# Performance work log

Measured on AMD Instinct MI355X. Metric: run time of the kernel, lower is better.

The kernel has to match this reference:

```python
import jax, jax.numpy as jnp
import numpy as np

N_NODES = 30000
N_EDGES = 300000
D_IN = 64
HID = 128
HEADS = 4
EDG = 2 * HID  # 256, num_edg_hiddens
OUT = 86
EPS = 1e-5
NEG_SLOPE = 0.2


def _kaiming(key, shape, fan_in):
    return jax.random.normal(key, shape, dtype=jnp.float32) * np.sqrt(2.0 / fan_in)


def _bn(x, w, b):
    # F.batch_norm(training=True): normalize with biased batch stats
    m = x.mean(axis=0)
    v = x.var(axis=0)
    return (x - m) / jnp.sqrt(v + EPS) * w + b


def _gat(x, src, dst, w, b, att_src, att_dst, n_nodes):
    # x: [N, Fin], w: [HEADS*HID, Fin] -> h: [N, HEADS, HID]
    h = (x @ w.T).reshape(x.shape[0], HEADS, -1)
    a_s = (h * att_src).sum(-1)  # [N, HEADS]
    a_d = (h * att_dst).sum(-1)  # [N, HEADS]
    alpha = jax.nn.leaky_relu(a_s[src] + a_d[dst], NEG_SLOPE)  # [E, HEADS]
    # segment softmax over destination node
    amax = jax.ops.segment_max(alpha, dst, num_segments=n_nodes)
    e = jnp.exp(alpha - amax[dst])
    denom = jax.ops.segment_sum(e, dst, num_segments=n_nodes)
    coef = e / denom[dst]  # [E, HEADS]
    out = jax.ops.segment_sum(h[src] * coef[:, :, None], dst, num_segments=n_nodes)
    return out.mean(axis=1) + b  # mean over heads (concat=False), [N, HID]


def setup_inputs() -> dict:
    key = jax.random.key(0)
    ks = jax.random.split(key, 16)
    x = jax.random.normal(ks[0], (N_NODES, D_IN), dtype=jnp.float32)
    edge_index = jax.random.randint(ks[1], (2, N_EDGES), 0, N_NODES, dtype=jnp.int32)
    return {
        'x': x,
        'edge_index': edge_index,
        'w0': _kaiming(ks[2], (HEADS * HID, D_IN), D_IN),
        'b0': jnp.zeros((HID,), jnp.float32),
        'ats0': _kaiming(ks[3], (1, HEADS, HID), HEADS * HID),
        'atd0': _kaiming(ks[4], (1, HEADS, HID), HEADS * HID),
        'bn1w': jnp.ones((HID,), jnp.float32),
        'bn1b': jnp.zeros((HID,), jnp.float32),
        'w2': _kaiming(ks[5], (HEADS * HID, HID), HID),
        'b2': jnp.zeros((HID,), jnp.float32),
        'ats1': _kaiming(ks[6], (1, HEADS, HID), HEADS * HID),
        'atd1': _kaiming(ks[7], (1, HEADS, HID), HEADS * HID),
        'bn2w': jnp.ones((HID,), jnp.float32),
        'bn2b': jnp.zeros((HID,), jnp.float32),
        'w4': _kaiming(ks[8], (EDG, EDG), EDG),
        'b4': jnp.zeros((EDG,), jnp.float32),
        'bn3w': jnp.ones((EDG,), jnp.float32),
        'bn3b': jnp.zeros((EDG,), jnp.float32),
        'w6': _kaiming(ks[9], (EDG, EDG), EDG),
        'b6': jnp.zeros((EDG,), jnp.float32),
        'bn4w': jnp.ones((EDG,), jnp.float32),
        'bn4b': jnp.zeros((EDG,), jnp.float32),
        'w8': _kaiming(ks[10], (OUT, EDG), EDG),
        'b8': jnp.zeros((OUT,), jnp.float32),
    }


def reference(x, edge_index, w0, b0, ats0, atd0, bn1w, bn1b, w2, b2, ats1, atd1,
              bn2w, bn2b, w4, b4, bn3w, bn3b, w6, b6, bn4w, bn4b, w8, b8):
    src, dst = edge_index[0], edge_index[1]
    n = x.shape[0]
    h = _gat(x, src, dst, w0, b0, ats0, atd0, n)
    x1 = jax.nn.relu(_bn(h, bn1w, bn1b))
    h = _gat(x1, src, dst, w2, b2, ats1, atd1, n)
    xr = jax.nn.relu(_bn(h, bn2w, bn2b) + x1)
    # edge feature MLP with residuals
    ef1 = jnp.concatenate([xr[src], xr[dst]], axis=1)  # [E, 2*HID]
    ef = _bn(ef1 @ w4.T + b4, bn3w, bn3b)
    ef1 = jax.nn.relu(ef + ef1)
    ef = _bn(ef1 @ w6.T + b6, bn4w, bn4b)
    ef = jax.nn.relu(ef + ef1)
    return ef @ w8.T + b8  # [E, OUT]
```

## Files before the change

kernel.cpp:

```cpp
#include <hip/hip_runtime.h>
#include <hip/hip_bf16.h>
#include <stdint.h>

typedef __hip_bfloat16 bf16;
typedef unsigned int u32;
typedef __attribute__((ext_vector_type(8))) short short8;
typedef __attribute__((ext_vector_type(4))) float f32x4;
typedef __attribute__((ext_vector_type(2))) float f32x2;

#define NNODES 30000
#define NEDGES 300000
#define NODE_PAD 30080
#define EDGE_PAD 300032
#define NCH128 2344
#define NEG_SLOPE 0.2f
#define BN_EPS 1e-5f
#define MAXD 128

__device__ __forceinline__ float b2f(short s) {
  u32 u = ((u32)(unsigned short)s) << 16;
  return __uint_as_float(u);
}
__device__ __forceinline__ short f2b(float f) {
  bf16 h = __float2bfloat16(f);
  return *(short*)&h;
}

__device__ __forceinline__ void gload16(const void* g, void* l) {
  __builtin_amdgcn_global_load_lds(
      (__attribute__((address_space(1))) unsigned int*)(uintptr_t)g,
      (__attribute__((address_space(3))) unsigned int*)(uintptr_t)l, 16, 0, 0);
}


__global__ void zfill(u32* __restrict__ p, int n) {
  int i = blockIdx.x * 256 + threadIdx.x;
  if (i < n) p[i] = 0u;
}

__global__ void fillpat(u32* __restrict__ p, u32 v, int n) {
  int i = blockIdx.x * 256 + threadIdx.x;
  if (i < n) p[i] = v;
}

__global__ void cvt_bf16_pad(const float* __restrict__ src, bf16* __restrict__ dst,
                             int rows_valid, int total, int cols) {
  int i = blockIdx.x * 256 + threadIdx.x;
  if (i >= total) return;
  int r = i / cols;
  float v = (r < rows_valid) ? src[i] : 0.f;
  dst[i] = __float2bfloat16(v);
}

__global__ void cvt_w45(const float* __restrict__ w4, bf16* __restrict__ w45b) {
  int i = blockIdx.x * 256 + threadIdx.x;
  if (i >= 512 * 128) return;
  int n = i >> 7, k = i & 127;
  float v = (n < 256) ? w4[n * 256 + k] : w4[(n - 256) * 256 + 128 + k];
  w45b[i] = __float2bfloat16(v);
}

__global__ void bn_coef(const float* __restrict__ stats, const float* __restrict__ w,
                        const float* __restrict__ b, int n, float invN,
                        float* __restrict__ sc, float* __restrict__ sh) {
  int c = threadIdx.x;
  if (c >= n) return;
  float m = stats[c] * invN;
  float var = stats[n + c] * invN - m * m;
  float rstd = rsqrtf(var + BN_EPS);
  sc[c] = rstd * w[c];
  sh[c] = b[c] - m * rstd * w[c];
}


__global__ void csr_hist(const int* __restrict__ ei, u32* __restrict__ cnt) {
  int e = blockIdx.x * 256 + threadIdx.x;
  if (e >= NEDGES) return;
  atomicAdd(&cnt[ei[NEDGES + e]], 1u);
}

__global__ __launch_bounds__(256) void scan30k(const u32* __restrict__ cnt,
                                               u32* __restrict__ rowptr) {
  __shared__ u32 part[256];
  int t = threadIdx.x;
  const int CH = (NNODES + 255) / 256;
  int i0 = t * CH;
  int i1 = i0 + CH;
  if (i1 > NNODES) i1 = NNODES;
  u32 s = 0;
  for (int i = i0; i < i1; ++i) s += cnt[i];
  part[t] = s;
  __syncthreads();
  for (int off = 1; off < 256; off <<= 1) {
    u32 v = (t >= off) ? part[t - off] : 0u;
    __syncthreads();
    part[t] += v;
    __syncthreads();
  }
  u32 run = (t == 0) ? 0u : part[t - 1];
  for (int i = i0; i < i1; ++i) {
    rowptr[i] = run;
    run += cnt[i];
  }
  if (t == 255) rowptr[NNODES] = run;
}

__global__ void csr_fill(const int* __restrict__ ei, const u32* __restrict__ rowptr,
                         u32* __restrict__ fill, u32* __restrict__ csrc) {
  int e = blockIdx.x * 256 + threadIdx.x;
  if (e >= NEDGES) return;
  int dst = ei[NEDGES + e];
  u32 pos = rowptr[dst] + atomicAdd(&fill[dst], 1u);
  csrc[pos] = (u32)ei[e];
}

__global__ __launch_bounds__(256) void gat_agg(
    const u32* __restrict__ rowptr, const u32* __restrict__ csrc,
    const float* __restrict__ a_s, const float* __restrict__ a_d,
    const bf16* __restrict__ hb, float* __restrict__ agg) {
  __shared__ float al[2][MAXD][4];
  __shared__ u32 srcl[2][MAXD];
  const int sub = threadIdx.x >> 7;
  const int d = threadIdx.x & 127;
  const int node = blockIdx.x * 2 + sub;
  u32 r0 = rowptr[node], r1 = rowptr[node + 1];
  int deg = (int)(r1 - r0);
  if (deg > MAXD) deg = MAXD;
  if (d < deg) {
    u32 s = csrc[r0 + d];
    srcl[sub][d] = s;
#pragma unroll
    for (int hh = 0; hh < 4; ++hh) {
      float a = a_s[s * 4 + hh] + a_d[node * 4 + hh];
      al[sub][d][hh] = (a > 0.f) ? a : NEG_SLOPE * a;
    }
  }
  __syncthreads();
  if (d < 4 && deg > 0) {
    float mx = -1e30f;
    for (int e = 0; e < deg; ++e) mx = fmaxf(mx, al[sub][e][d]);
    float sum = 0.f;
    for (int e = 0; e < deg; ++e) {
      float v = __expf(al[sub][e][d] - mx);
      al[sub][e][d] = v;
      sum += v;
    }
    float inv = 1.f / sum;
    for (int e = 0; e < deg; ++e) al[sub][e][d] *= inv;
  }
  __syncthreads();
  float acc = 0.f;
  const short* hp = (const short*)hb;
#pragma unroll 1
  for (int e = 0; e < deg; ++e) {
    u32 s = srcl[sub][e];
    const short* row = hp + (size_t)s * 512 + d;
    f32x4 c = *(const f32x4*)&al[sub][e][0];
    acc += c[0] * b2f(row[0]) + c[1] * b2f(row[128]) +
           c[2] * b2f(row[256]) + c[3] * b2f(row[384]);
  }
  agg[(size_t)node * 128 + d] = acc * 0.25f;
}

__global__ __launch_bounds__(256) void gemm_bt(
    const bf16* __restrict__ A, const bf16* __restrict__ B, bf16* __restrict__ Cout,
    int K, int ldc, int Mvalid, int Nvalid) {
  __shared__ __align__(16) short smA[2][128 * 64];
  __shared__ __align__(16) short smB[2][128 * 64];
  const int tid = threadIdx.x;
  const int lane = tid & 63;
  const int wid = tid >> 6;
  const int wr = wid >> 1, wc = wid & 1;
  const size_t arow0 = (size_t)blockIdx.x * 128;
  const size_t brow0 = (size_t)blockIdx.y * 128;
  f32x4 acc[4][4] = {};
  const int nk = K >> 6;

  int srow[4], scol[4];
#pragma unroll
  for (int i = 0; i < 4; ++i) {
    int s = i * 256 + tid;
    srow[i] = s >> 3;
    scol[i] = ((s & 7) ^ ((s >> 3) & 7)) * 8;
  }
  auto stage = [&](int buf, int kt) {
#pragma unroll
    for (int i = 0; i < 4; ++i) {
      int s = i * 256 + tid;
      gload16(A + (arow0 + srow[i]) * K + kt * 64 + scol[i], &smA[buf][s * 8]);
      gload16(B + (brow0 + srow[i]) * K + kt * 64 + scol[i], &smB[buf][s * 8]);
    }
  };
  auto compute = [&](int buf) {
#pragma unroll
    for (int ks = 0; ks < 2; ++ks) {
      short8 af[4], bfr[4];
      const int cg = ks * 4 + (lane >> 4);
#pragma unroll
      for (int m = 0; m < 4; ++m) {
        int row = wr * 64 + m * 16 + (lane & 15);
        af[m] = *(const short8*)&smA[buf][row * 64 + ((cg ^ (row & 7)) << 3)];
      }
#pragma unroll
      for (int n = 0; n < 4; ++n) {
        int row = wc * 64 + n * 16 + (lane & 15);
        bfr[n] = *(const short8*)&smB[buf][row * 64 + ((cg ^ (row & 7)) << 3)];
      }
#pragma unroll
      for (int m = 0; m < 4; ++m)
#pragma unroll
        for (int n = 0; n < 4; ++n)
          acc[m][n] = __builtin_amdgcn_mfma_f32_16x16x32_bf16(af[m], bfr[n], acc[m][n], 0, 0, 0);
    }
  };

  stage(0, 0);
  __syncthreads();
  int cur = 0;
  for (int kt = 0; kt < nk; ++kt) {
    if (kt + 1 < nk) stage(cur ^ 1, kt + 1);
    compute(cur);
    __syncthreads();
    cur ^= 1;
  }

  const int rbase = (int)arow0 + wr * 64 + (lane >> 4) * 4;
  const int cbase = (int)brow0 + wc * 64 + (lane & 15);
#pragma unroll
  for (int m = 0; m < 4; ++m) {
#pragma unroll
    for (int n = 0; n < 4; ++n) {
      int col = cbase + n * 16;
      if (col >= Nvalid) continue;
#pragma unroll
      for (int r = 0; r < 4; ++r) {
        int row = rbase + m * 16 + r;
        if (row < Mvalid)
          Cout[(size_t)row * ldc + col] = __float2bfloat16(acc[m][n][r]);
      }
    }
  }
}

__global__ __launch_bounds__(512, 2) void gemm2_v8(
    const bf16* __restrict__ A, const bf16* __restrict__ Bw, bf16* __restrict__ C,
    float* __restrict__ statsOut) {
  __shared__ __align__(16) short smA[2][128 * 256];
  const int tid = threadIdx.x;
  const int lane = tid & 63;
  const int wid = tid >> 6;
  const int lr = lane & 15, lk = lane >> 4;

  short8 bfrag[2][8];
#pragma unroll
  for (int n = 0; n < 2; ++n)
#pragma unroll
    for (int ks = 0; ks < 8; ++ks)
      bfrag[n][ks] = *(const short8*)(Bw + (size_t)(wid * 32 + n * 16 + lr) * 256 + (ks * 4 + lk) * 8);

  auto stage = [&](int buf, int chunk) {
    const bf16* Ab = A + (size_t)chunk * 128 * 256;
#pragma unroll
    for (int i = 0; i < 8; ++i) {
      int s = i * 512 + tid;
      int p = s >> 10;
      int row = (s >> 3) & 127;
      int c8 = s & 7;
      gload16(Ab + row * 256 + (p * 8 + (c8 ^ (row & 7))) * 8, &smA[buf][s * 8]);
    }
  };

  float ss[2] = {}, sq[2] = {};

  auto compute = [&](int buf, int chunk) {
    f32x4 acc[8][2];
#pragma unroll
    for (int g = 0; g < 8; ++g) { acc[g][0] = {}; acc[g][1] = {}; }
#pragma unroll
    for (int ks = 0; ks < 8; ++ks) {
      const int p = ks >> 1;
      const int cgl = (ks & 1) * 4 + lk;
#pragma unroll
      for (int g = 0; g < 8; ++g) {
        int row = g * 16 + lr;
        short8 af = *(const short8*)&smA[buf][p * 8192 + row * 64 + ((cgl ^ (row & 7)) << 3)];
        acc[g][0] = __builtin_amdgcn_mfma_f32_16x16x32_bf16(af, bfrag[0][ks], acc[g][0], 0, 0, 0);
        acc[g][1] = __builtin_amdgcn_mfma_f32_16x16x32_bf16(af, bfrag[1][ks], acc[g][1], 0, 0, 0);
      }
    }
    size_t rbase = (size_t)chunk * 128;
#pragma unroll
    for (int g = 0; g < 8; ++g) {
#pragma unroll
      for (int n = 0; n < 2; ++n) {
        int col = wid * 32 + n * 16 + lr;
#pragma unroll
        for (int j = 0; j < 4; ++j) {
          float v = acc[g][n][j];
          ss[n] += v;
          sq[n] += v * v;
          C[(rbase + g * 16 + lk * 4 + j) * 256 + col] = __float2bfloat16(v);
        }
      }
    }
  };

  int c = blockIdx.x;
  stage(0, c);
  __syncthreads();
  int buf = 0;
  while (true) {
    int nx = c + (int)gridDim.x;
    if (nx < NCH128) stage(buf ^ 1, nx);
    compute(buf, c);
    if (nx >= NCH128) break;
    __syncthreads();
    buf ^= 1;
    c = nx;
  }

#pragma unroll
  for (int n = 0; n < 2; ++n) {
    float s = ss[n], q = sq[n];
    s += __shfl_xor(s, 16); s += __shfl_xor(s, 32);
    q += __shfl_xor(q, 16); q += __shfl_xor(q, 32);
    if (lk == 0) {
      atomicAdd(&statsOut[wid * 32 + n * 16 + lr], s);
      atomicAdd(&statsOut[256 + wid * 32 + n * 16 + lr], q);
    }
  }
}

__global__ __launch_bounds__(256, 2) void gemm3_v3(
    const bf16* __restrict__ Y, const bf16* __restrict__ E, const bf16* __restrict__ Bw,
    float* __restrict__ Cout, const float* __restrict__ scf, const float* __restrict__ shf,
    const float* __restrict__ bias) {
  __shared__ __align__(16) short smW[96 * 256];
  __shared__ __align__(16) short smA[64 * 256];
  const int tid = threadIdx.x;
  const int lane = tid & 63;
  const int wid = tid >> 6;
  const int lr = lane & 15, lk = lane >> 4;

#pragma unroll
  for (int i = 0; i < 12; ++i) {
    int s = i * 256 + tid;
    int row = s >> 5, c8 = s & 31;
    gload16(Bw + row * 256 + (c8 ^ (row & 7)) * 8, &smW[s * 8]);
  }

  const int cb = (tid & 31) * 8;
  f32x4 sc0 = *(const f32x4*)&scf[cb];
  f32x4 sc1 = *(const f32x4*)&scf[cb + 4];
  f32x4 sh0 = *(const f32x4*)&shf[cb];
  f32x4 sh1 = *(const f32x4*)&shf[cb + 4];
  float bb[6][4];
#pragma unroll
  for (int f = 0; f < 6; ++f)
#pragma unroll
    for (int r = 0; r < 4; ++r) {
      int n = f * 16 + lk * 4 + r;
      bb[f][r] = (n < 86) ? bias[n] : 0.f;
    }

  short8 y[8], e[8];
  auto loadYE = [&](int t) {
    size_t base = (size_t)t * 64 * 256;
#pragma unroll
    for (int j = 0; j < 8; ++j) {
      size_t off = base + (size_t)(j * 256 + tid) * 8;
      y[j] = *(const short8*)(Y + off);
      e[j] = *(const short8*)(E + off);
    }
  };

  const int NT = EDGE_PAD / 64;
  int t = blockIdx.x;
  loadYE(t);
  __syncthreads();

  while (true) {
#pragma unroll
    for (int j = 0; j < 8; ++j) {
      int s = j * 256 + tid;
      int row = s >> 5, c8 = s & 31;
      short8 o;
#pragma unroll
      for (int jj = 0; jj < 4; ++jj) {
        o[jj]     = f2b(fmaxf(b2f(y[j][jj]) * sc0[jj] + sh0[jj] + b2f(e[j][jj]), 0.f));
        o[jj + 4] = f2b(fmaxf(b2f(y[j][jj + 4]) * sc1[jj] + sh1[jj] + b2f(e[j][jj + 4]), 0.f));
      }
      *(short8*)&smA[row * 256 + ((c8 ^ (row & 7)) << 3)] = o;
    }
    __syncthreads();
    int cur = t;
    int nx = t + (int)gridDim.x;
    if (nx < NT) loadYE(nx);

    f32x4 acc[6] = {};
#pragma unroll
    for (int ks = 0; ks < 8; ++ks) {
      int cg = ks * 4 + lk;
      int ra = wid * 16 + lr;
      short8 af = *(const short8*)&smA[ra * 256 + ((cg ^ (ra & 7)) << 3)];
#pragma unroll
      for (int f = 0; f < 6; ++f) {
        int rw = f * 16 + lr;
        short8 wf = *(const short8*)&smW[rw * 256 + ((cg ^ (rw & 7)) << 3)];
        acc[f] = __builtin_amdgcn_mfma_f32_16x16x32_bf16(wf, af, acc[f], 0, 0, 0);
      }
    }

    int rbase = cur * 64 + wid * 16;
    if (rbase < NEDGES) {
      float* gp = Cout + (size_t)(rbase + lr) * 86;
#pragma unroll
      for (int f = 0; f < 6; ++f) {
        int n0 = f * 16 + lk * 4;
        if (n0 + 1 < 86) {
          f32x2 v;
          v[0] = acc[f][0] + bb[f][0];
          v[1] = acc[f][1] + bb[f][1];
          *(f32x2*)(gp + n0) = v;
        }
        if (n0 + 3 < 86) {
          f32x2 v;
          v[0] = acc[f][2] + bb[f][2];
          v[1] = acc[f][3] + bb[f][3];
          *(f32x2*)(gp + n0 + 2) = v;
        }
      }
    }
    if (nx >= NT) break;
    t = nx;
    __syncthreads();
  }
}


__global__ __launch_bounds__(256) void att_reduce(
    const bf16* __restrict__ h, const float* __restrict__ ats, const float* __restrict__ atd,
    float* __restrict__ a_s, float* __restrict__ a_d) {
  int n = blockIdx.x;
  int lane = threadIdx.x & 63;
  int hd = threadIdx.x >> 6;
  const bf16* hp = h + (size_t)n * 512 + hd * 128;
  const float* sw = ats + hd * 128;
  const float* dw = atd + hd * 128;
  float h1 = __bfloat162float(hp[lane]), h2 = __bfloat162float(hp[lane + 64]);
  float s = h1 * sw[lane] + h2 * sw[lane + 64];
  float d = h1 * dw[lane] + h2 * dw[lane + 64];
#pragma unroll
  for (int off = 32; off > 0; off >>= 1) {
    s += __shfl_down(s, off);
    d += __shfl_down(d, off);
  }
  if (lane == 0) {
    a_s[n * 4 + hd] = s;
    a_d[n * 4 + hd] = d;
  }
}


__global__ __launch_bounds__(256) void col_stats128(const float* __restrict__ X,
                                                    float* __restrict__ stats, int rows) {
  __shared__ float smS[8][128], smQ[8][128];
  int t = threadIdx.x;
  int sub = t >> 5;
  int c4 = (t & 31) * 4;
  int rend = blockIdx.x * 64 + 64;
  if (rend > rows) rend = rows;
  f32x4 s = {}, q = {};
  for (int r = blockIdx.x * 64 + sub; r < rend; r += 8) {
    f32x4 v = *(const f32x4*)&X[(size_t)r * 128 + c4];
    s += v;
    q += v * v;
  }
  *(f32x4*)&smS[sub][c4] = s;
  *(f32x4*)&smQ[sub][c4] = q;
  __syncthreads();
  if (t < 128) {
    float ts = 0.f, tq = 0.f;
#pragma unroll
    for (int g = 0; g < 8; ++g) { ts += smS[g][t]; tq += smQ[g][t]; }
    atomicAdd(&stats[t], ts);
    atomicAdd(&stats[128 + t], tq);
  }
}

__global__ void bn_relu_node(const float* __restrict__ agg, const float* __restrict__ stats,
                             const float* __restrict__ w, const float* __restrict__ b,
                             bf16* __restrict__ xout) {
  int i = blockIdx.x * 256 + threadIdx.x;
  if (i >= NODE_PAD * 128) return;
  int r = i >> 7, c = i & 127;
  float v = 0.f;
  if (r < NNODES) {
    float m = stats[c] * (1.f / NNODES);
    float var = stats[128 + c] * (1.f / NNODES) - m * m;
    float rstd = rsqrtf(var + BN_EPS);
    v = fmaxf((agg[i] - m) * rstd * w[c] + b[c], 0.f);
  }
  xout[i] = __float2bfloat16(v);
}

__global__ void bn_res_relu_node(const float* __restrict__ agg, const float* __restrict__ stats,
                                 const float* __restrict__ w, const float* __restrict__ b,
                                 const bf16* __restrict__ x1b, bf16* __restrict__ xrb) {
  int i = blockIdx.x * 256 + threadIdx.x;
  if (i >= NODE_PAD * 128) return;
  int r = i >> 7, c = i & 127;
  float v = 0.f;
  if (r < NNODES) {
    float m = stats[c] * (1.f / NNODES);
    float var = stats[128 + c] * (1.f / NNODES) - m * m;
    float rstd = rsqrtf(var + BN_EPS);
    v = fmaxf((agg[i] - m) * rstd * w[c] + b[c] + __bfloat162float(x1b[i]), 0.f);
  }
  xrb[i] = __float2bfloat16(v);
}

__device__ __forceinline__ void accum_nw(short8 pa, short8 qa, f32x4& s0, f32x4& s1,
                                         f32x4& q0, f32x4& q1) {
  float v[8];
#pragma unroll
  for (int j = 0; j < 8; ++j) v[j] = b2f(pa[j]) + b2f(qa[j]);
  s0[0] += v[0]; s0[1] += v[1]; s0[2] += v[2]; s0[3] += v[3];
  s1[0] += v[4]; s1[1] += v[5]; s1[2] += v[6]; s1[3] += v[7];
  q0[0] += v[0] * v[0]; q0[1] += v[1] * v[1]; q0[2] += v[2] * v[2]; q0[3] += v[3] * v[3];
  q1[0] += v[4] * v[4]; q1[1] += v[5] * v[5]; q1[2] += v[6] * v[6]; q1[3] += v[7] * v[7];
}

__global__ __launch_bounds__(256) void e_stats_nw(const int* __restrict__ ei,
                                                  const bf16* __restrict__ PQ,
                                                  float* __restrict__ stats) {
  __shared__ float smS[8][256], smQ[8][256];
  int t = threadIdx.x;
  int sub = t >> 5;
  int c8 = (t & 31) * 8;
  int ebase = blockIdx.x * 128 + sub * 16;
  f32x4 s0 = {}, s1 = {}, q0 = {}, q1 = {};
#pragma unroll 1
  for (int i = 0; i < 16; i += 4) {
    int e = ebase + i;
    if (e + 3 < NEDGES) {
      int4 sn = *(const int4*)&ei[e];
      int4 dn = *(const int4*)&ei[NEDGES + e];
      short8 p0 = *(const short8*)&PQ[(size_t)sn.x * 512 + c8];
      short8 p1 = *(const short8*)&PQ[(size_t)sn.y * 512 + c8];
      short8 p2 = *(const short8*)&PQ[(size_t)sn.z * 512 + c8];
      short8 p3 = *(const short8*)&PQ[(size_t)sn.w * 512 + c8];
      short8 r0 = *(const short8*)&PQ[(size_t)dn.x * 512 + 256 + c8];
      short8 r1 = *(const short8*)&PQ[(size_t)dn.y * 512 + 256 + c8];
      short8 r2 = *(const short8*)&PQ[(size_t)dn.z * 512 + 256 + c8];
      short8 r3 = *(const short8*)&PQ[(size_t)dn.w * 512 + 256 + c8];
      accum_nw(p0, r0, s0, s1, q0, q1);
      accum_nw(p1, r1, s0, s1, q0, q1);
      accum_nw(p2, r2, s0, s1, q0, q1);
      accum_nw(p3, r3, s0, s1, q0, q1);
    } else {
      for (int j = 0; j < 4; ++j) {
        int ej = e + j;
        if (ej >= NEDGES) break;
        int sn = ei[ej], dn = ei[NEDGES + ej];
        short8 p = *(const short8*)&PQ[(size_t)sn * 512 + c8];
        short8 r = *(const short8*)&PQ[(size_t)dn * 512 + 256 + c8];
        accum_nw(p, r, s0, s1, q0, q1);
      }
    }
  }
  *(f32x4*)&smS[sub][c8] = s0;
  *(f32x4*)&smS[sub][c8 + 4] = s1;
  *(f32x4*)&smQ[sub][c8] = q0;
  *(f32x4*)&smQ[sub][c8 + 4] = q1;
  __syncthreads();
  float ts = 0.f, tq = 0.f;
#pragma unroll
  for (int g = 0; g < 8; ++g) { ts += smS[g][t]; tq += smQ[g][t]; }
  atomicAdd(&stats[t], ts);
  atomicAdd(&stats[256 + t], tq);
}

__global__ __launch_bounds__(256) void ef2_direct(const int* __restrict__ ei,
                                                  const bf16* __restrict__ PQ,
                                                  const bf16* __restrict__ xrb,
                                                  const float* __restrict__ sc3,
                                                  const float* __restrict__ sh3,
                                                  bf16* __restrict__ ef2) {
  int t = threadIdx.x;
  int e = blockIdx.x * 8 + (t >> 5);
  int c8 = (t & 31) * 8;
  size_t base = (size_t)e * 256 + c8;
  short8 out = {};
  if (e < NEDGES) {
    int sn = ei[e], dn = ei[NEDGES + e];
    short8 p = *(const short8*)&PQ[(size_t)sn * 512 + c8];
    short8 q = *(const short8*)&PQ[(size_t)dn * 512 + 256 + c8];
    int node = (c8 < 128) ? sn : dn;
    short8 res = *(const short8*)&xrb[(size_t)node * 128 + (c8 & 127)];
    f32x4 scl = *(const f32x4*)&sc3[c8];
    f32x4 sch = *(const f32x4*)&sc3[c8 + 4];
    f32x4 shl = *(const f32x4*)&sh3[c8];
    f32x4 shh = *(const f32x4*)&sh3[c8 + 4];
#pragma unroll
    for (int j = 0; j < 4; ++j) {
      float v0 = (b2f(p[j]) + b2f(q[j])) * scl[j] + shl[j] + b2f(res[j]);
      float v1 = (b2f(p[j + 4]) + b2f(q[j + 4])) * sch[j] + shh[j] + b2f(res[j + 4]);
      out[j] = f2b(fmaxf(v0, 0.f));
      out[j + 4] = f2b(fmaxf(v1, 0.f));
    }
  }
  *(short8*)&ef2[base] = out;
}


extern "C" void kernel_launch(void* const* d_in, const int* in_sizes, int n_in,
                              void* d_out, int out_size, void* d_ws, size_t ws_size,
                              hipStream_t stream) {
  const float* x    = (const float*)d_in[0];
  const int*   ei   = (const int*)d_in[1];
  const float* w0   = (const float*)d_in[2];
  const float* ats0 = (const float*)d_in[4];
  const float* atd0 = (const float*)d_in[5];
  const float* bn1w = (const float*)d_in[6];
  const float* bn1b = (const float*)d_in[7];
  const float* w2   = (const float*)d_in[8];
  const float* ats1 = (const float*)d_in[10];
  const float* atd1 = (const float*)d_in[11];
  const float* bn2w = (const float*)d_in[12];
  const float* bn2b = (const float*)d_in[13];
  const float* w4   = (const float*)d_in[14];
  const float* bn3w = (const float*)d_in[16];
  const float* bn3b = (const float*)d_in[17];
  const float* w6   = (const float*)d_in[18];
  const float* bn4w = (const float*)d_in[20];
  const float* bn4b = (const float*)d_in[21];
  const float* w8   = (const float*)d_in[22];
  const float* b8   = (const float*)d_in[23];

  const size_t REG = 153616384;
  char* ws = (char*)d_ws;
  bf16*  ef2b = (bf16*)ws;
  char*  R    = ws + REG;
  bf16*  hb    = (bf16*)(R);
  bf16*  xb    = (bf16*)(R + 61603840);
  bf16*  x1b   = (bf16*)(R + 65454080);
  bf16*  xrb   = (bf16*)(R + 73154560);
  float* a_s   = (float*)(R + 80855040);
  float* a_d   = (float*)(R + 81335040);
  u32*   rowptr= (u32*)  (R + 81815040);
  u32*   cntf  = (u32*)  (R + 82295040);
  u32*   csrc  = (u32*)  (R + 82775040);
  float* agg   = (float*)(R + 87575040);
  bf16*  PQ    = hb;
  bf16*  y2b   = (bf16*)R;
  char*  S     = ws + 2 * REG;
  bf16*  w0b   = (bf16*)(S);
  bf16*  w2b   = (bf16*)(S + 65536);
  bf16*  w45b  = (bf16*)(S + 196608);
  bf16*  w6b   = (bf16*)(S + 327680);
  bf16*  w8pb  = (bf16*)(S + 458752);
  float* stats1= (float*)(S + 524288);
  float* stats2= (float*)(S + 526336);
  float* sc2   = (float*)(S + 528384);
  float* sh2   = (float*)(S + 529408);
  float* sc3   = (float*)(S + 530432);
  float* sh3   = (float*)(S + 531456);
  const size_t needed = 2 * REG + 532480;
  if (ws_size < needed) {
    fillpat<<<(out_size + 255) / 256, 256, 0, stream>>>((u32*)d_out, 0x7F7F7F7Fu, out_size);
    return;
  }

  cvt_bf16_pad<<<(NODE_PAD * 64 + 255) / 256, 256, 0, stream>>>(x, xb, NNODES, NODE_PAD * 64, 64);
  cvt_bf16_pad<<<(512 * 64 + 255) / 256, 256, 0, stream>>>(w0, w0b, 512, 512 * 64, 64);
  cvt_bf16_pad<<<(512 * 128 + 255) / 256, 256, 0, stream>>>(w2, w2b, 512, 512 * 128, 128);
  cvt_w45<<<(512 * 128 + 255) / 256, 256, 0, stream>>>(w4, w45b);
  cvt_bf16_pad<<<(256 * 256 + 255) / 256, 256, 0, stream>>>(w6, w6b, 256, 256 * 256, 256);
  cvt_bf16_pad<<<(128 * 256 + 255) / 256, 256, 0, stream>>>(w8, w8pb, 86, 128 * 256, 256);

  const int eb = (NEDGES + 255) / 256;

  zfill<<<(NNODES + 255) / 256, 256, 0, stream>>>(cntf, NNODES);
  csr_hist<<<eb, 256, 0, stream>>>(ei, cntf);
  scan30k<<<1, 256, 0, stream>>>(cntf, rowptr);
  zfill<<<(NNODES + 255) / 256, 256, 0, stream>>>(cntf, NNODES);
  csr_fill<<<eb, 256, 0, stream>>>(ei, rowptr, cntf, csrc);

  gemm_bt<<<dim3(NODE_PAD / 128, 4), 256, 0, stream>>>(xb, w0b, hb, 64, 512, NODE_PAD, 512);
  att_reduce<<<NNODES, 256, 0, stream>>>(hb, ats0, atd0, a_s, a_d);
  gat_agg<<<NNODES / 2, 256, 0, stream>>>(rowptr, csrc, a_s, a_d, hb, agg);
  zfill<<<1, 256, 0, stream>>>((u32*)stats1, 256);
  col_stats128<<<(NNODES + 63) / 64, 256, 0, stream>>>(agg, stats1, NNODES);
  bn_relu_node<<<NODE_PAD * 128 / 256, 256, 0, stream>>>(agg, stats1, bn1w, bn1b, x1b);

  gemm_bt<<<dim3(NODE_PAD / 128, 4), 256, 0, stream>>>(x1b, w2b, hb, 128, 512, NODE_PAD, 512);
  att_reduce<<<NNODES, 256, 0, stream>>>(hb, ats1, atd1, a_s, a_d);
  gat_agg<<<NNODES / 2, 256, 0, stream>>>(rowptr, csrc, a_s, a_d, hb, agg);
  zfill<<<1, 256, 0, stream>>>((u32*)stats1, 256);
  col_stats128<<<(NNODES + 63) / 64, 256, 0, stream>>>(agg, stats1, NNODES);
  bn_res_relu_node<<<NODE_PAD * 128 / 256, 256, 0, stream>>>(agg, stats1, bn2w, bn2b, x1b, xrb);

  gemm_bt<<<dim3(NODE_PAD / 128, 4), 256, 0, stream>>>(xrb, w45b, PQ, 128, 512, NODE_PAD, 512);
  zfill<<<2, 256, 0, stream>>>((u32*)stats1, 512);
  e_stats_nw<<<(NEDGES + 127) / 128, 256, 0, stream>>>(ei, PQ, stats1);
  bn_coef<<<1, 256, 0, stream>>>(stats1, bn3w, bn3b, 256, 1.f / NEDGES, sc3, sh3);
  ef2_direct<<<EDGE_PAD / 8, 256, 0, stream>>>(ei, PQ, xrb, sc3, sh3, ef2b);
  zfill<<<2, 256, 0, stream>>>((u32*)stats2, 512);
  gemm2_v8<<<586, 512, 0, stream>>>(ef2b, w6b, y2b, stats2);
  bn_coef<<<1, 256, 0, stream>>>(stats2, bn4w, bn4b, 256, 1.f / NEDGES, sc2, sh2);
  gemm3_v3<<<2344, 256, 0, stream>>>(y2b, ef2b, w8pb, (float*)d_out, sc2, sh2, b8);
}
```

Baseline: 691.4 us.

## Restructure final GEMM with register-resident weights, 128-row tiles and double-buffered LDS

```diff
diff --git a/kernel.cpp b/kernel.cpp
--- a/kernel.cpp
+++ b/kernel.cpp
@@ -70,6 +70,18 @@
   float rstd = rsqrtf(var + BN_EPS);
   sc[c] = rstd * w[c];
   sh[c] = b[c] - m * rstd * w[c];
+}
+
+__global__ void bn_coef_b(const float* __restrict__ stats, const float* __restrict__ w,
+                          const float* __restrict__ b, int n, float invN,
+                          bf16* __restrict__ sc, bf16* __restrict__ sh) {
+  int c = threadIdx.x;
+  if (c >= n) return;
+  float m = stats[c] * invN;
+  float var = stats[n + c] * invN - m * m;
+  float rstd = rsqrtf(var + BN_EPS);
+  sc[c] = __float2bfloat16(rstd * w[c]);
+  sh[c] = __float2bfloat16(b[c] - m * rstd * w[c]);
 }
 
 
@@ -331,109 +343,129 @@
   }
 }
 
-__global__ __launch_bounds__(256, 2) void gemm3_v3(
-    const bf16* __restrict__ Y, const bf16* __restrict__ E, const bf16* __restrict__ Bw,
-    float* __restrict__ Cout, const float* __restrict__ scf, const float* __restrict__ shf,
+__global__ __launch_bounds__(512, 2) void gemm3_v4(
+    const bf16* __restrict__ Y, const bf16* __restrict__ E, const bf16* __restrict__ W8g,
+    float* __restrict__ Cout, const bf16* __restrict__ scb, const bf16* __restrict__ shb,
     const float* __restrict__ bias) {
-  __shared__ __align__(16) short smW[96 * 256];
-  __shared__ __align__(16) short smA[64 * 256];
+  __shared__ __align__(16) short smA[2][128 * 256];
   const int tid = threadIdx.x;
   const int lane = tid & 63;
   const int wid = tid >> 6;
   const int lr = lane & 15, lk = lane >> 4;
-
-#pragma unroll
-  for (int i = 0; i < 12; ++i) {
-    int s = i * 256 + tid;
-    int row = s >> 5, c8 = s & 31;
-    gload16(Bw + row * 256 + (c8 ^ (row & 7)) * 8, &smW[s * 8]);
-  }
-
-  const int cb = (tid & 31) * 8;
-  f32x4 sc0 = *(const f32x4*)&scf[cb];
-  f32x4 sc1 = *(const f32x4*)&scf[cb + 4];
-  f32x4 sh0 = *(const f32x4*)&shf[cb];
-  f32x4 sh1 = *(const f32x4*)&shf[cb + 4];
-  float bb[6][4];
-#pragma unroll
-  for (int f = 0; f < 6; ++f)
+  const int g2 = wid & 3;
+  const int fh = wid >> 2;
+
+  short8 wf[3][8];
+#pragma unroll
+  for (int ff = 0; ff < 3; ++ff)
+#pragma unroll
+    for (int ks = 0; ks < 8; ++ks)
+      wf[ff][ks] = *(const short8*)(W8g + (size_t)((fh * 3 + ff) * 16 + lr) * 256 + (ks * 4 + lk) * 8);
+
+  const int xo = (tid & 7) ^ ((tid >> 3) & 7);
+  short8 csc[4], csh[4];
+#pragma unroll
+  for (int p = 0; p < 4; ++p) {
+    csc[p] = *(const short8*)((const short*)scb + (p * 8 + xo) * 8);
+    csh[p] = *(const short8*)((const short*)shb + (p * 8 + xo) * 8);
+  }
+  float bb[3][4];
+#pragma unroll
+  for (int ff = 0; ff < 3; ++ff)
 #pragma unroll
     for (int r = 0; r < 4; ++r) {
-      int n = f * 16 + lk * 4 + r;
-      bb[f][r] = (n < 86) ? bias[n] : 0.f;
+      int n = (fh * 3 + ff) * 16 + lk * 4 + r;
+      bb[ff][r] = (n < 86) ? bias[n] : 0.f;
     }
 
   short8 y[8], e[8];
   auto loadYE = [&](int t) {
-    size_t base = (size_t)t * 64 * 256;
+    const bf16* Yb = Y + (size_t)t * 128 * 256;
+    const bf16* Eb = E + (size_t)t * 128 * 256;
 #pragma unroll
     for (int j = 0; j < 8; ++j) {
-      size_t off = base + (size_t)(j * 256 + tid) * 8;
-      y[j] = *(const short8*)(Y + off);
-      e[j] = *(const short8*)(E + off);
+      int s = j * 512 + tid;
+      int p = s >> 10;
+      int row = (s >> 3) & 127;
+      int c8 = s & 7;
+      size_t off = (size_t)row * 256 + (p * 8 + (c8 ^ (row & 7))) * 8;
+      y[j] = *(const short8*)(Yb + off);
+      e[j] = *(const short8*)(Eb + off);
     }
   };
-
-  const int NT = EDGE_PAD / 64;
-  int t = blockIdx.x;
-  loadYE(t);
+  auto fuseWrite = [&](int buf) {
+#pragma unroll
+    for (int j = 0; j < 8; ++j) {
+      int s = j * 512 + tid;
+      int pp = j >> 1;
+      short8 o;
+#pragma unroll
+      for (int jj = 0; jj < 8; ++jj) {
+        float v = b2f(y[j][jj]) * b2f(csc[pp][jj]) + b2f(csh[pp][jj]) + b2f(e[j][jj]);
+        o[jj] = f2b(fmaxf(v, 0.f));
+      }
+      *(short8*)&smA[buf][s * 8] = o;
+    }
+  };
+
+  auto compute = [&](int buf, int cur) {
+    f32x4 acc[2][3];
+#pragma unroll
+    for (int g = 0; g < 2; ++g)
+#pragma unroll
+      for (int ff = 0; ff < 3; ++ff) acc[g][ff] = {};
+#pragma unroll
+    for (int ks = 0; ks < 8; ++ks) {
+      const int p = ks >> 1;
+      const int cgl = (ks & 1) * 4 + lk;
+#pragma unroll
+      for (int g = 0; g < 2; ++g) {
+        int ra = g2 * 32 + g * 16 + lr;
+        short8 af = *(const short8*)&smA[buf][p * 8192 + ra * 64 + ((cgl ^ (ra & 7)) << 3)];
+#pragma unroll
+        for (int ff = 0; ff < 3; ++ff)
+          acc[g][ff] = __builtin_amdgcn_mfma_f32_16x16x32_bf16(wf[ff][ks], af, acc[g][ff], 0, 0, 0);
+      }
+    }
+#pragma unroll
+    for (int g = 0; g < 2; ++g) {
+      int rb = cur * 128 + g2 * 32 + g * 16;
+      if (rb < NEDGES) {
+        float* gp = Cout + (size_t)(rb + lr) * 86;
+#pragma unroll
+        for (int ff = 0; ff < 3; ++ff) {
+          int n0 = (fh * 3 + ff) * 16 + lk * 4;
+          if (n0 + 1 < 86) {
+            f32x2 v;
+            v[0] = acc[g][ff][0] + bb[ff][0];
+            v[1] = acc[g][ff][1] + bb[ff][1];
+            *(f32x2*)(gp + n0) = v;
+          }
+          if (n0 + 3 < 86) {
+            f32x2 v;
+            v[0] = acc[g][ff][2] + bb[ff][2];
+            v[1] = acc[g][ff][3] + bb[ff][3];
+            *(f32x2*)(gp + n0 + 2) = v;
+          }
+        }
+      }
+    }
+  };
+
+  int c = blockIdx.x;
+  int buf = 0;
+  loadYE(c);
+  fuseWrite(buf);
   __syncthreads();
-
   while (true) {
-#pragma unroll
-    for (int j = 0; j < 8; ++j) {
-      int s = j * 256 + tid;
-      int row = s >> 5, c8 = s & 31;
-      short8 o;
-#pragma unroll
-      for (int jj = 0; jj < 4; ++jj) {
-        o[jj]     = f2b(fmaxf(b2f(y[j][jj]) * sc0[jj] + sh0[jj] + b2f(e[j][jj]), 0.f));
-        o[jj + 4] = f2b(fmaxf(b2f(y[j][jj + 4]) * sc1[jj] + sh1[jj] + b2f(e[j][jj + 4]), 0.f));
-      }
-      *(short8*)&smA[row * 256 + ((c8 ^ (row & 7)) << 3)] = o;
-    }
+    int nx = c + (int)gridDim.x;
+    if (nx < NCH128) loadYE(nx);
+    compute(buf, c);
+    if (nx >= NCH128) break;
+    fuseWrite(buf ^ 1);
     __syncthreads();
-    int cur = t;
-    int nx = t + (int)gridDim.x;
-    if (nx < NT) loadYE(nx);
-
-    f32x4 acc[6] = {};
-#pragma unroll
-    for (int ks = 0; ks < 8; ++ks) {
-      int cg = ks * 4 + lk;
-      int ra = wid * 16 + lr;
-      short8 af = *(const short8*)&smA[ra * 256 + ((cg ^ (ra & 7)) << 3)];
-#pragma unroll
-      for (int f = 0; f < 6; ++f) {
-        int rw = f * 16 + lr;
-        short8 wf = *(const short8*)&smW[rw * 256 + ((cg ^ (rw & 7)) << 3)];
-        acc[f] = __builtin_amdgcn_mfma_f32_16x16x32_bf16(wf, af, acc[f], 0, 0, 0);
-      }
-    }
-
-    int rbase = cur * 64 + wid * 16;
-    if (rbase < NEDGES) {
-      float* gp = Cout + (size_t)(rbase + lr) * 86;
-#pragma unroll
-      for (int f = 0; f < 6; ++f) {
-        int n0 = f * 16 + lk * 4;
-        if (n0 + 1 < 86) {
-          f32x2 v;
-          v[0] = acc[f][0] + bb[f][0];
-          v[1] = acc[f][1] + bb[f][1];
-          *(f32x2*)(gp + n0) = v;
-        }
-        if (n0 + 3 < 86) {
-          f32x2 v;
-          v[0] = acc[f][2] + bb[f][2];
-          v[1] = acc[f][3] + bb[f][3];
-          *(f32x2*)(gp + n0 + 2) = v;
-        }
-      }
-    }
-    if (nx >= NT) break;
-    t = nx;
-    __syncthreads();
+    buf ^= 1;
+    c = nx;
   }
 }
 
@@ -662,11 +694,11 @@
   bf16*  w8pb  = (bf16*)(S + 458752);
   float* stats1= (float*)(S + 524288);
   float* stats2= (float*)(S + 526336);
-  float* sc2   = (float*)(S + 528384);
-  float* sh2   = (float*)(S + 529408);
-  float* sc3   = (float*)(S + 530432);
-  float* sh3   = (float*)(S + 531456);
-  const size_t needed = 2 * REG + 532480;
+  bf16*  scb2  = (bf16*)(S + 528384);
+  bf16*  shb2  = (bf16*)(S + 528896);
+  float* sc3   = (float*)(S + 529408);
+  float* sh3   = (float*)(S + 530432);
+  const size_t needed = 2 * REG + 531456;
   if (ws_size < needed) {
     fillpat<<<(out_size + 255) / 256, 256, 0, stream>>>((u32*)d_out, 0x7F7F7F7Fu, out_size);
     return;
@@ -708,6 +740,6 @@
   ef2_direct<<<EDGE_PAD / 8, 256, 0, stream>>>(ei, PQ, xrb, sc3, sh3, ef2b);
   zfill<<<2, 256, 0, stream>>>((u32*)stats2, 512);
   gemm2_v8<<<586, 512, 0, stream>>>(ef2b, w6b, y2b, stats2);
-  bn_coef<<<1, 256, 0, stream>>>(stats2, bn4w, bn4b, 256, 1.f / NEDGES, sc2, sh2);
-  gemm3_v3<<<2344, 256, 0, stream>>>(y2b, ef2b, w8pb, (float*)d_out, sc2, sh2, b8);
-}
+  bn_coef_b<<<1, 256, 0, stream>>>(stats2, bn4w, bn4b, 256, 1.f / NEDGES, scb2, shb2);
+  gemm3_v4<<<1172, 512, 0, stream>>>(y2b, ef2b, w8pb, (float*)d_out, scb2, shb2, b8);
+}
```

After: 786.2 us. 1.14x slower.
